# Kernel tuning notes

Hardware: AMD Instinct MI355X
Metric: run time of the kernel (lower is better)

## Reference

```python
import jax, jax.numpy as jnp
import numpy as np

NUM_GROUPS = 8
EPS = 1e-5


def group_norm(x, scale, bias):
    # x: [b, c, h, w]; 8 groups, affine, eps=1e-5 (torch GroupNorm defaults)
    b, c, h, w = x.shape
    xg = x.reshape(b, NUM_GROUPS, c // NUM_GROUPS * h * w)
    mean = jnp.mean(xg, axis=-1, keepdims=True)
    var = jnp.var(xg, axis=-1, keepdims=True)
    xg = (xg - mean) * jax.lax.rsqrt(var + EPS)
    x = xg.reshape(b, c, h, w)
    return x * scale[None, :, None, None] + bias[None, :, None, None]


def conv1x1(x, w, bias):
    # 1x1 conv == per-pixel linear: x [b,c,h,w], w [c_out,c_in], bias [c_out]
    return jnp.einsum('oc,bchw->bohw', w, x) + bias[None, :, None, None]


def setup_inputs() -> dict:
    key = jax.random.key(0)
    ks = jax.random.split(key, 11)
    b, c, h, w = 8, 512, 32, 32
    init = 1.0 / np.sqrt(c)
    d = {
        'x': jax.random.normal(ks[0], (b, c, h, w), dtype=jnp.float32),
        'gn_scale': jnp.ones((c,), jnp.float32),
        'gn_bias': jnp.zeros((c,), jnp.float32),
        'wq': jax.random.uniform(ks[1], (c, c), jnp.float32, -init, init),
        'bq': jax.random.uniform(ks[2], (c,), jnp.float32, -init, init),
        'wk': jax.random.uniform(ks[3], (c, c), jnp.float32, -init, init),
        'bk': jax.random.uniform(ks[4], (c,), jnp.float32, -init, init),
        'wv': jax.random.uniform(ks[5], (c, c), jnp.float32, -init, init),
        'bv': jax.random.uniform(ks[6], (c,), jnp.float32, -init, init),
        'wproj': jax.random.uniform(ks[7], (c, c), jnp.float32, -init, init),
        'bproj': jax.random.uniform(ks[8], (c,), jnp.float32, -init, init),
    }
    return d


def reference(x, gn_scale, gn_bias, wq, bq, wk, bk, wv, bv, wproj, bproj):
    b, c, h, w = x.shape
    h_ = group_norm(x, gn_scale, gn_bias)
    q = conv1x1(h_, wq, bq).reshape(b, c, h * w)  # [b,c,hw]
    k = conv1x1(h_, wk, bk).reshape(b, c, h * w)
    v = conv1x1(h_, wv, bv).reshape(b, c, h * w)
    scale = 1.0 / np.sqrt(c).astype(np.float32)
    # scores[b,i,j] = sum_c q[b,c,i]*k[b,c,j]
    scores = jnp.einsum('bci,bcj->bij', q, k) * scale
    attn = jax.nn.softmax(scores, axis=2)  # softmax over j (keys)
    # h_[b,c,i] = sum_j v[b,c,j] * attn[b,i,j]
    out = jnp.einsum('bcj,bij->bci', v, attn).reshape(b, c, h, w)
    out = conv1x1(out, wproj, bproj)
    return x + out
```

## Files before the change

### kernel.cpp

```cpp
#include <hip/hip_runtime.h>
#include <hip/hip_bf16.h>

#define DI __device__ __forceinline__

typedef __bf16 bf16x8 __attribute__((ext_vector_type(8)));
typedef float f32x4 __attribute__((ext_vector_type(4)));

typedef const void __attribute__((address_space(1))) gas_t;
typedef void __attribute__((address_space(3))) las_t;

DI unsigned short f2bf(float f) {
    unsigned u = __builtin_bit_cast(unsigned, f);
    u += 0x7fffu + ((u >> 16) & 1u);
    return (unsigned short)(u >> 16);
}

__global__ __launch_bounds__(256) void prep_kernel(const float* __restrict__ x,
                                                   float2* __restrict__ part,
                                                   const float* __restrict__ w0,
                                                   const float* __restrict__ w1,
                                                   const float* __restrict__ w2,
                                                   const float* __restrict__ w3,
                                                   unsigned short* __restrict__ wb) {
    int bx = blockIdx.x;
    int t = threadIdx.x;
    if (bx < 512) {
        int b = bx & 7, g = (bx >> 3) & 7, ch = bx >> 6;
        size_t base = ((size_t)b * 512 + g * 64 + ch * 8) * 1024;
        const float4* xp = (const float4*)(x + base);
        float s = 0.f, q = 0.f;
#pragma unroll
        for (int it = 0; it < 8; ++it) {
            float4 v = xp[it * 256 + t];
            s += (v.x + v.y) + (v.z + v.w);
            q += (v.x * v.x + v.y * v.y) + (v.z * v.z + v.w * v.w);
        }
#pragma unroll
        for (int o = 32; o; o >>= 1) { s += __shfl_xor(s, o); q += __shfl_xor(q, o); }
        __shared__ float rs[4], rq[4];
        int lane = t & 63, wid = t >> 6;
        if (!lane) { rs[wid] = s; rq[wid] = q; }
        __syncthreads();
        if (t == 0)
            part[((b * 8 + g) * 8) + ch] =
                make_float2(rs[0] + rs[1] + rs[2] + rs[3],
                            rq[0] + rq[1] + rq[2] + rq[3]);
    } else {
        int idx4 = bx - 512;
        int w = idx4 >> 8;
        const float* s = (w == 0) ? w0 : (w == 1) ? w1 : (w == 2) ? w2 : w3;
        unsigned short* o = wb + (size_t)w * 262144;
        int idx = (idx4 & 255) * 256 + t;
        float4 v = ((const float4*)s)[idx];
        ushort4 r;
        r.x = f2bf(v.x); r.y = f2bf(v.y); r.z = f2bf(v.z); r.w = f2bf(v.w);
        ((ushort4*)o)[idx] = r;
    }
}

__global__ __launch_bounds__(256) void gn_applyT(const float* __restrict__ x,
                                                 const float2* __restrict__ part,
                                                 const float* __restrict__ gs,
                                                 const float* __restrict__ gb,
                                                 unsigned short* __restrict__ hT) {
    int bx = blockIdx.x;
    int b = bx & 7, g = (bx >> 3) & 7, ic = bx >> 6;
    int bg = b * 8 + g;
    float s = 0.f, q = 0.f;
#pragma unroll
    for (int k = 0; k < 8; ++k) { float2 p = part[bg * 8 + k]; s += p.x; q += p.y; }
    float mean = s * (1.f / 65536.f);
    float var = q * (1.f / 65536.f) - mean * mean;
    float rstd = rsqrtf(var + 1e-5f);

    __shared__ unsigned short tile[128 * 66];
    int t = threadIdx.x;
    int i4 = t & 31, cq = t >> 5;
    size_t xbase = ((size_t)b * 512 + g * 64) * 1024 + ic * 128;
#pragma unroll
    for (int pass = 0; pass < 8; ++pass) {
        int c = pass * 8 + cq;
        float4 v = *(const float4*)&x[xbase + (size_t)c * 1024 + i4 * 4];
        int gc = g * 64 + c;
        float sc = gs[gc] * rstd, bi = gb[gc] - mean * sc;
        unsigned short* tp = &tile[(i4 * 4) * 66 + c];
        tp[0]   = f2bf(v.x * sc + bi);
        tp[66]  = f2bf(v.y * sc + bi);
        tp[132] = f2bf(v.z * sc + bi);
        tp[198] = f2bf(v.w * sc + bi);
    }
    __syncthreads();
    int i = t >> 1, h = t & 1;
    const unsigned short* tp2 = &tile[i * 66 + h * 32];
    unsigned short* op = &hT[(size_t)b * (1024 * 512) + (size_t)(ic * 128 + i) * 512 + g * 64 + h * 32];
#pragma unroll
    for (int cc = 0; cc < 4; ++cc) {
        unsigned short tmp[8];
#pragma unroll
        for (int j = 0; j < 8; ++j) tmp[j] = tp2[cc * 8 + j];
        *(uint4*)&op[cc * 8] = *(const uint4*)tmp;
    }
}

template <int ROWS>
DI void stage_tile(const unsigned short* __restrict__ g, int ldK,
                   unsigned short* lds, int t) {
    int row_in = t >> 3;
    int kg = (t & 7) ^ (row_in & 7);
    const unsigned short* src = g + (size_t)row_in * ldK + kg * 8;
    unsigned short* dst = lds + ((t >> 6) << 9);
#pragma unroll
    for (int c = 0; c < ROWS / 32; ++c) {
        __builtin_amdgcn_global_load_lds(
            (gas_t*)(unsigned long long)(src + (size_t)c * 32 * ldK),
            (las_t*)(unsigned)(unsigned long long)(dst + c * 2048),
            16, 0, 0);
    }
}

DI bf16x8 frag(const unsigned short* lds, int r, int kg) {
    return *(const bf16x8*)((const char*)lds + r * 128 + ((kg ^ (r & 7)) << 4));
}

template <int MR>
DI void compute_step(const unsigned short* As_, const unsigned short* Bs_,
                     f32x4 (&acc)[MR][4], int wm, int wn, int l15, int lks) {
#pragma unroll
    for (int kk = 0; kk < 2; ++kk) {
        bf16x8 a_[MR], b_[4];
#pragma unroll
        for (int m = 0; m < MR; ++m) a_[m] = frag(As_, wm + m * 16 + l15, kk * 4 + lks);
#pragma unroll
        for (int n = 0; n < 4; ++n) b_[n] = frag(Bs_, wn + n * 16 + l15, kk * 4 + lks);
#pragma unroll
        for (int m = 0; m < MR; ++m)
#pragma unroll
            for (int n = 0; n < 4; ++n)
                acc[m][n] = __builtin_amdgcn_mfma_f32_16x16x32_bf16(a_[m], b_[n], acc[m][n], 0, 0, 0);
    }
}

template <int TM, int MODE, int MINW, int PIPE>
__global__ __launch_bounds__(256, MINW) void gemm_bt(
        const unsigned short* __restrict__ A, const unsigned short* __restrict__ B,
        const float* __restrict__ b0, const float* __restrict__ b1,
        const float* __restrict__ b2,
        void* __restrict__ C0, void* __restrict__ C1, void* __restrict__ C2,
        const float* __restrict__ resid, float* __restrict__ spart,
        int M, int N, int K, float scale, size_t sA, size_t sB, size_t sC) {
    constexpr int MR = TM / 32;
    constexpr int NBUF = PIPE ? 2 : 1;
    __shared__ __align__(16) unsigned short As[NBUF][TM * 64];
    __shared__ __align__(16) unsigned short Bs[NBUF][128 * 64];
    int bx = blockIdx.x;
    int b = bx & 7;
    int tile = bx >> 3;
    int nTx = N >> 7;
    int tx = tile % nTx, ty = tile / nTx;
    int m0 = ty * TM, n0 = tx << 7;
    const unsigned short* Ag = A + sA * b + (size_t)m0 * K;
    const unsigned short* Bg = B + sB * b + (size_t)n0 * K;
    int t = threadIdx.x;
    int lane = t & 63, wid = t >> 6;
    int wm = (wid >> 1) * (TM / 2), wn = (wid & 1) * 64;
    const int l15 = lane & 15, lks = lane >> 4;

    f32x4 acc[MR][4];
#pragma unroll
    for (int i = 0; i < MR; ++i)
#pragma unroll
        for (int j = 0; j < 4; ++j) acc[i][j] = (f32x4){0.f, 0.f, 0.f, 0.f};

    float inv[4];
    if constexpr (MODE == 2) {
#pragma unroll
        for (int n = 0; n < 4; ++n) {
            int ng = n0 + wn + n * 16 + l15;
            float ssum = 0.f;
#pragma unroll
            for (int k = 0; k < 16; ++k) ssum += spart[(size_t)(b * 16 + k) * 1024 + ng];
            inv[n] = 1.f / ssum;
        }
    }
    float bn4[4];
    if constexpr (MODE == 3) {
#pragma unroll
        for (int n = 0; n < 4; ++n) bn4[n] = b0[n0 + wn + n * 16 + l15];
    }

    if constexpr (PIPE == 0) {
        for (int k0 = 0; k0 < K; k0 += 64) {
            stage_tile<TM>(Ag + k0, K, &As[0][0], t);
            stage_tile<128>(Bg + k0, K, &Bs[0][0], t);
            asm volatile("s_waitcnt vmcnt(0)" ::: "memory");
            __syncthreads();
            compute_step<MR>(&As[0][0], &Bs[0][0], acc, wm, wn, l15, lks);
            __syncthreads();
        }
    } else {
        stage_tile<TM>(Ag, K, &As[0][0], t);
        stage_tile<128>(Bg, K, &Bs[0][0], t);
        asm volatile("s_waitcnt vmcnt(0)" ::: "memory");
        __syncthreads();
        int cur = 0;
        for (int k0 = 0; k0 < K; k0 += 64) {
            if (k0 + 64 < K) {
                stage_tile<TM>(Ag + k0 + 64, K, &As[cur ^ 1][0], t);
                stage_tile<128>(Bg + k0 + 64, K, &Bs[cur ^ 1][0], t);
            }
            compute_step<MR>(&As[cur][0], &Bs[cur][0], acc, wm, wn, l15, lks);
            if (k0 + 64 < K) {
                asm volatile("s_waitcnt vmcnt(0)" ::: "memory");
                __syncthreads();
            }
            cur ^= 1;
        }
    }

    const int rbase = lks * 4;
    const size_t cb = sC * b;
    if constexpr (MODE == 0) {
        if (m0 < 1024) {
            unsigned short* Ct = (unsigned short*)(m0 < 512 ? C0 : C1) + cb;
            const float* bias = (m0 < 512) ? b0 : b1;
            int moff = (m0 < 512) ? 0 : 512;
#pragma unroll
            for (int m = 0; m < MR; ++m) {
                int mg = m0 - moff + wm + m * 16 + rbase;
                float bv4[4];
#pragma unroll
                for (int j = 0; j < 4; ++j) bv4[j] = bias[mg + j];
#pragma unroll
                for (int n = 0; n < 4; ++n) {
                    int ng = n0 + wn + n * 16 + l15;
                    f32x4 v = acc[m][n];
                    ushort4 o;
                    o.x = f2bf(v[0] + bv4[0]); o.y = f2bf(v[1] + bv4[1]);
                    o.z = f2bf(v[2] + bv4[2]); o.w = f2bf(v[3] + bv4[3]);
                    *(ushort4*)&Ct[(size_t)ng * 512 + mg] = o;
                }
            }
        } else {
            unsigned short* Vb = (unsigned short*)C2 + cb;
#pragma unroll
            for (int m = 0; m < MR; ++m) {
                int mg = m0 - 1024 + wm + m * 16 + rbase;
                float bv4[4];
#pragma unroll
                for (int j = 0; j < 4; ++j) bv4[j] = b2[mg + j];
#pragma unroll
                for (int n = 0; n < 4; ++n) {
                    int ng = n0 + wn + n * 16 + l15;
                    f32x4 v = acc[m][n];
#pragma unroll
                    for (int j = 0; j < 4; ++j)
                        Vb[(size_t)(mg + j) * 1024 + ng] = f2bf(v[j] + bv4[j]);
                }
            }
        }
    } else if constexpr (MODE == 1) {
        unsigned short* Ct = (unsigned short*)C0 + cb;
        float psum[4] = {0.f, 0.f, 0.f, 0.f};
#pragma unroll
        for (int m = 0; m < MR; ++m) {
            int mg = m0 + wm + m * 16 + rbase;
#pragma unroll
            for (int n = 0; n < 4; ++n) {
                int ng = n0 + wn + n * 16 + l15;
                f32x4 v = acc[m][n];
                float e0 = __expf(v[0] * scale), e1 = __expf(v[1] * scale);
                float e2 = __expf(v[2] * scale), e3 = __expf(v[3] * scale);
                psum[n] += (e0 + e1) + (e2 + e3);
                ushort4 o;
                o.x = f2bf(e0); o.y = f2bf(e1); o.z = f2bf(e2); o.w = f2bf(e3);
                *(ushort4*)&Ct[(size_t)ng * M + mg] = o;
            }
        }
        int rb = (m0 >> 7) * 2 + (wid >> 1);
#pragma unroll
        for (int n = 0; n < 4; ++n) {
            float p = psum[n];
            p += __shfl_xor(p, 16);
            p += __shfl_xor(p, 32);
            if (lks == 0) {
                int ng = n0 + wn + n * 16 + l15;
                spart[(size_t)(b * 16 + rb) * 1024 + ng] = p;
            }
        }
    } else if constexpr (MODE == 2) {
        unsigned short* Ct = (unsigned short*)C0 + cb;
#pragma unroll
        for (int m = 0; m < MR; ++m) {
            int mg = m0 + wm + m * 16 + rbase;
#pragma unroll
            for (int n = 0; n < 4; ++n) {
                int ng = n0 + wn + n * 16 + l15;
                f32x4 v = acc[m][n];
                ushort4 o;
                o.x = f2bf(v[0] * inv[n]); o.y = f2bf(v[1] * inv[n]);
                o.z = f2bf(v[2] * inv[n]); o.w = f2bf(v[3] * inv[n]);
                *(ushort4*)&Ct[(size_t)ng * M + mg] = o;
            }
        }
    } else {
        float* Cf = (float*)C0 + cb;
#pragma unroll
        for (int m = 0; m < MR; ++m) {
            int mg = m0 + wm + m * 16 + rbase;
#pragma unroll
            for (int n = 0; n < 4; ++n) {
                int ng = n0 + wn + n * 16 + l15;
                f32x4 v = acc[m][n];
                const float* rp = resid + cb + (size_t)ng * M + mg;
                float4 o;
                o.x = v[0] + bn4[n] + rp[0]; o.y = v[1] + bn4[n] + rp[1];
                o.z = v[2] + bn4[n] + rp[2]; o.w = v[3] + bn4[n] + rp[3];
                *(float4*)&Cf[(size_t)ng * M + mg] = o;
            }
        }
    }
}

extern "C" void kernel_launch(void* const* d_in, const int* in_sizes, int n_in,
                              void* d_out, int out_size, void* d_ws, size_t ws_size,
                              hipStream_t stream) {
    const float* x  = (const float*)d_in[0];
    const float* gs = (const float*)d_in[1];
    const float* gb = (const float*)d_in[2];
    const float* wq = (const float*)d_in[3];
    const float* bq = (const float*)d_in[4];
    const float* wk = (const float*)d_in[5];
    const float* bk = (const float*)d_in[6];
    const float* wv = (const float*)d_in[7];
    const float* bv = (const float*)d_in[8];
    const float* wp = (const float*)d_in[9];
    const float* bp = (const float*)d_in[10];
    float* out = (float*)d_out;

    char* ws = (char*)d_ws;
    const size_t MB = 1u << 20;
    unsigned short* hT = (unsigned short*)(ws + 0);
    unsigned short* wb = (unsigned short*)(ws + 8 * MB);
    unsigned short* qT = (unsigned short*)(ws + 10 * MB);
    unsigned short* kT = (unsigned short*)(ws + 18 * MB);
    unsigned short* vN = (unsigned short*)(ws + 26 * MB);
    unsigned short* E  = (unsigned short*)(ws + 34 * MB);
    unsigned short* OT = (unsigned short*)(ws + 50 * MB);
    float2* gnpart     = (float2*)(ws + 58 * MB);
    float*  spart      = (float*)(ws + 58 * MB + 65536);

    const unsigned short* wpb = wb + 3 * 262144;
    const size_t sH = 1024 * 512;
    const size_t sS = 1024 * 1024;

    prep_kernel<<<1536, 256, 0, stream>>>(x, gnpart, wq, wk, wv, wp, wb);
    gn_applyT<<<512, 256, 0, stream>>>(x, gnpart, gs, gb, hT);

    gemm_bt<128, 0, 3, 0><<<96 * 8, 256, 0, stream>>>(
        wb, hT, bq, bk, bv, qT, kT, vN, nullptr, nullptr,
        1536, 1024, 512, 1.f, 0, sH, sH);
    gemm_bt<128, 1, 2, 1><<<64 * 8, 256, 0, stream>>>(
        kT, qT, nullptr, nullptr, nullptr, E, nullptr, nullptr, nullptr, spart,
        1024, 1024, 512, 0.044194173824159216f, sH, sH, sS);
    gemm_bt<64, 2, 2, 1><<<64 * 8, 256, 0, stream>>>(
        vN, E, nullptr, nullptr, nullptr, OT, nullptr, nullptr, nullptr, spart,
        512, 1024, 1024, 1.f, sH, sS, sH);
    gemm_bt<64, 3, 2, 1><<<64 * 8, 256, 0, stream>>>(
        OT, wpb, bp, nullptr, nullptr, out, nullptr, nullptr, x, nullptr,
        1024, 512, 512, 1.f, sH, 0, (size_t)512 * 1024);
}
```

Baseline: 75.79 us.

## Fuse all stages into one cooperative persistent kernel with grid syncs

Replaces the six separate launches with a single cooperative kernel of 512 blocks that runs group-norm statistics with weight conversion, the normalize-transpose, and the four GEMM phases in sequence, separated by grid-wide barriers. The QKV projection is retiled to 192-row tiles so its work fits the fixed 512-block grid, and the weight conversion is folded into the stats blocks. The aim is to remove launch gaps and tail idle time between kernels. In exchange it adds grid-sync overhead, needs an occupancy of two blocks per CU, and limits each phase to the fixed grid size. The old multi-kernel path remains as a fallback.

```diff
diff --git a/kernel.cpp b/kernel.cpp
--- a/kernel.cpp
+++ b/kernel.cpp
@@ -1,5 +1,8 @@
 #include <hip/hip_runtime.h>
 #include <hip/hip_bf16.h>
+#include <hip/hip_cooperative_groups.h>
+
+namespace cg = cooperative_groups;
 
 #define DI __device__ __forceinline__
 
@@ -15,55 +18,258 @@
     return (unsigned short)(u >> 16);
 }
 
-__global__ __launch_bounds__(256) void prep_kernel(const float* __restrict__ x,
-                                                   float2* __restrict__ part,
-                                                   const float* __restrict__ w0,
-                                                   const float* __restrict__ w1,
-                                                   const float* __restrict__ w2,
-                                                   const float* __restrict__ w3,
-                                                   unsigned short* __restrict__ wb) {
-    int bx = blockIdx.x;
-    int t = threadIdx.x;
-    if (bx < 512) {
-        int b = bx & 7, g = (bx >> 3) & 7, ch = bx >> 6;
-        size_t base = ((size_t)b * 512 + g * 64 + ch * 8) * 1024;
-        const float4* xp = (const float4*)(x + base);
-        float s = 0.f, q = 0.f;
-#pragma unroll
-        for (int it = 0; it < 8; ++it) {
-            float4 v = xp[it * 256 + t];
-            s += (v.x + v.y) + (v.z + v.w);
-            q += (v.x * v.x + v.y * v.y) + (v.z * v.z + v.w * v.w);
-        }
-#pragma unroll
-        for (int o = 32; o; o >>= 1) { s += __shfl_xor(s, o); q += __shfl_xor(q, o); }
-        __shared__ float rs[4], rq[4];
-        int lane = t & 63, wid = t >> 6;
-        if (!lane) { rs[wid] = s; rq[wid] = q; }
+template <int ROWS>
+DI void stage_tile(const unsigned short* __restrict__ g, int ldK,
+                   unsigned short* lds, int t) {
+    int row_in = t >> 3;
+    int kg = (t & 7) ^ (row_in & 7);
+    const unsigned short* src = g + (size_t)row_in * ldK + kg * 8;
+    unsigned short* dst = lds + ((t >> 6) << 9);
+#pragma unroll
+    for (int c = 0; c < ROWS / 32; ++c) {
+        __builtin_amdgcn_global_load_lds(
+            (gas_t*)(unsigned long long)(src + (size_t)c * 32 * ldK),
+            (las_t*)(unsigned)(unsigned long long)(dst + c * 2048),
+            16, 0, 0);
+    }
+}
+
+DI bf16x8 frag(const unsigned short* lds, int r, int kg) {
+    return *(const bf16x8*)((const char*)lds + r * 128 + ((kg ^ (r & 7)) << 4));
+}
+
+template <int MR>
+DI void compute_step(const unsigned short* As_, const unsigned short* Bs_,
+                     f32x4 (&acc)[MR][4], int wm, int wn, int l15, int lks) {
+#pragma unroll
+    for (int kk = 0; kk < 2; ++kk) {
+        bf16x8 a_[MR], b_[4];
+#pragma unroll
+        for (int m = 0; m < MR; ++m) a_[m] = frag(As_, wm + m * 16 + l15, kk * 4 + lks);
+#pragma unroll
+        for (int n = 0; n < 4; ++n) b_[n] = frag(Bs_, wn + n * 16 + l15, kk * 4 + lks);
+#pragma unroll
+        for (int m = 0; m < MR; ++m)
+#pragma unroll
+            for (int n = 0; n < 4; ++n)
+                acc[m][n] = __builtin_amdgcn_mfma_f32_16x16x32_bf16(a_[m], b_[n], acc[m][n], 0, 0, 0);
+    }
+}
+
+template <int TM, int MODE, int PIPE>
+DI void gemm_phase(unsigned short* AsB, unsigned short* BsB,
+                   const unsigned short* __restrict__ A, const unsigned short* __restrict__ B,
+                   const float* __restrict__ b0, const float* __restrict__ b1,
+                   const float* __restrict__ b2,
+                   void* __restrict__ C0, void* __restrict__ C1, void* __restrict__ C2,
+                   const float* __restrict__ resid, float* __restrict__ spart,
+                   int M, int N, int K, float scale, size_t sA, size_t sB, size_t sC,
+                   int bx, int t) {
+    constexpr int MR = TM / 32;
+    constexpr int ABUF = TM * 64;
+    constexpr int BBUF = 128 * 64;
+    int b = bx & 7;
+    int tile = bx >> 3;
+    int nTx = N >> 7;
+    int tx = tile % nTx, ty = tile / nTx;
+    int m0 = ty * TM, n0 = tx << 7;
+    const unsigned short* Ag = A + sA * b + (size_t)m0 * K;
+    const unsigned short* Bg = B + sB * b + (size_t)n0 * K;
+    int lane = t & 63, wid = t >> 6;
+    int wm = (wid >> 1) * (TM / 2), wn = (wid & 1) * 64;
+    const int l15 = lane & 15, lks = lane >> 4;
+
+    f32x4 acc[MR][4];
+#pragma unroll
+    for (int i = 0; i < MR; ++i)
+#pragma unroll
+        for (int j = 0; j < 4; ++j) acc[i][j] = (f32x4){0.f, 0.f, 0.f, 0.f};
+
+    float inv[4];
+    if constexpr (MODE == 2) {
+#pragma unroll
+        for (int n = 0; n < 4; ++n) {
+            int ng = n0 + wn + n * 16 + l15;
+            float ssum = 0.f;
+#pragma unroll
+            for (int k = 0; k < 16; ++k) ssum += spart[(size_t)(b * 16 + k) * 1024 + ng];
+            inv[n] = 1.f / ssum;
+        }
+    }
+    float bn4[4];
+    if constexpr (MODE == 3) {
+#pragma unroll
+        for (int n = 0; n < 4; ++n) bn4[n] = b0[n0 + wn + n * 16 + l15];
+    }
+
+    if constexpr (PIPE == 0) {
+        for (int k0 = 0; k0 < K; k0 += 64) {
+            stage_tile<TM>(Ag + k0, K, AsB, t);
+            stage_tile<128>(Bg + k0, K, BsB, t);
+            asm volatile("s_waitcnt vmcnt(0)" ::: "memory");
+            __syncthreads();
+            compute_step<MR>(AsB, BsB, acc, wm, wn, l15, lks);
+            __syncthreads();
+        }
+    } else {
+        stage_tile<TM>(Ag, K, AsB, t);
+        stage_tile<128>(Bg, K, BsB, t);
+        asm volatile("s_waitcnt vmcnt(0)" ::: "memory");
         __syncthreads();
-        if (t == 0)
-            part[((b * 8 + g) * 8) + ch] =
-                make_float2(rs[0] + rs[1] + rs[2] + rs[3],
-                            rq[0] + rq[1] + rq[2] + rq[3]);
+        int cur = 0;
+        for (int k0 = 0; k0 < K; k0 += 64) {
+            if (k0 + 64 < K) {
+                stage_tile<TM>(Ag + k0 + 64, K, AsB + (cur ^ 1) * ABUF, t);
+                stage_tile<128>(Bg + k0 + 64, K, BsB + (cur ^ 1) * BBUF, t);
+            }
+            compute_step<MR>(AsB + cur * ABUF, BsB + cur * BBUF, acc, wm, wn, l15, lks);
+            if (k0 + 64 < K) {
+                asm volatile("s_waitcnt vmcnt(0)" ::: "memory");
+                __syncthreads();
+            }
+            cur ^= 1;
+        }
+    }
+
+    const int rbase = lks * 4;
+    const size_t cb = sC * b;
+    if constexpr (MODE == 0) {
+#pragma unroll
+        for (int m = 0; m < MR; ++m) {
+            int mgg = m0 + wm + m * 16 + rbase;
+            int region = mgg >> 9;
+            int local = mgg & 511;
+            const float* bias = (region == 0) ? b0 : (region == 1) ? b1 : b2;
+            float bv4[4];
+#pragma unroll
+            for (int j = 0; j < 4; ++j) bv4[j] = bias[local + j];
+            if (region < 2) {
+                unsigned short* Ct = (unsigned short*)(region == 0 ? C0 : C1) + cb;
+#pragma unroll
+                for (int n = 0; n < 4; ++n) {
+                    int ng = n0 + wn + n * 16 + l15;
+                    f32x4 v = acc[m][n];
+                    ushort4 o;
+                    o.x = f2bf(v[0] + bv4[0]); o.y = f2bf(v[1] + bv4[1]);
+                    o.z = f2bf(v[2] + bv4[2]); o.w = f2bf(v[3] + bv4[3]);
+                    *(ushort4*)&Ct[(size_t)ng * 512 + local] = o;
+                }
+            } else {
+                unsigned short* Vb = (unsigned short*)C2 + cb;
+#pragma unroll
+                for (int n = 0; n < 4; ++n) {
+                    int ng = n0 + wn + n * 16 + l15;
+                    f32x4 v = acc[m][n];
+#pragma unroll
+                    for (int j = 0; j < 4; ++j)
+                        Vb[(size_t)(local + j) * 1024 + ng] = f2bf(v[j] + bv4[j]);
+                }
+            }
+        }
+    } else if constexpr (MODE == 1) {
+        unsigned short* Ct = (unsigned short*)C0 + cb;
+        float psum[4] = {0.f, 0.f, 0.f, 0.f};
+#pragma unroll
+        for (int m = 0; m < MR; ++m) {
+            int mg = m0 + wm + m * 16 + rbase;
+#pragma unroll
+            for (int n = 0; n < 4; ++n) {
+                int ng = n0 + wn + n * 16 + l15;
+                f32x4 v = acc[m][n];
+                float e0 = __expf(v[0] * scale), e1 = __expf(v[1] * scale);
+                float e2 = __expf(v[2] * scale), e3 = __expf(v[3] * scale);
+                psum[n] += (e0 + e1) + (e2 + e3);
+                ushort4 o;
+                o.x = f2bf(e0); o.y = f2bf(e1); o.z = f2bf(e2); o.w = f2bf(e3);
+                *(ushort4*)&Ct[(size_t)ng * M + mg] = o;
+            }
+        }
+        int rb = (m0 >> 7) * 2 + (wid >> 1);
+#pragma unroll
+        for (int n = 0; n < 4; ++n) {
+            float p = psum[n];
+            p += __shfl_xor(p, 16);
+            p += __shfl_xor(p, 32);
+            if (lks == 0) {
+                int ng = n0 + wn + n * 16 + l15;
+                spart[(size_t)(b * 16 + rb) * 1024 + ng] = p;
+            }
+        }
+    } else if constexpr (MODE == 2) {
+        unsigned short* Ct = (unsigned short*)C0 + cb;
+#pragma unroll
+        for (int m = 0; m < MR; ++m) {
+            int mg = m0 + wm + m * 16 + rbase;
+#pragma unroll
+            for (int n = 0; n < 4; ++n) {
+                int ng = n0 + wn + n * 16 + l15;
+                f32x4 v = acc[m][n];
+                ushort4 o;
+                o.x = f2bf(v[0] * inv[n]); o.y = f2bf(v[1] * inv[n]);
+                o.z = f2bf(v[2] * inv[n]); o.w = f2bf(v[3] * inv[n]);
+                *(ushort4*)&Ct[(size_t)ng * M + mg] = o;
+            }
+        }
     } else {
-        int idx4 = bx - 512;
-        int w = idx4 >> 8;
-        const float* s = (w == 0) ? w0 : (w == 1) ? w1 : (w == 2) ? w2 : w3;
+        float* Cf = (float*)C0 + cb;
+#pragma unroll
+        for (int m = 0; m < MR; ++m) {
+            int mg = m0 + wm + m * 16 + rbase;
+#pragma unroll
+            for (int n = 0; n < 4; ++n) {
+                int ng = n0 + wn + n * 16 + l15;
+                f32x4 v = acc[m][n];
+                const float* rp = resid + cb + (size_t)ng * M + mg;
+                float4 o;
+                o.x = v[0] + bn4[n] + rp[0]; o.y = v[1] + bn4[n] + rp[1];
+                o.z = v[2] + bn4[n] + rp[2]; o.w = v[3] + bn4[n] + rp[3];
+                *(float4*)&Cf[(size_t)ng * M + mg] = o;
+            }
+        }
+    }
+}
+
+DI void stats_wcvt_body(const float* __restrict__ x, float2* __restrict__ part,
+                        const float* __restrict__ w0, const float* __restrict__ w1,
+                        const float* __restrict__ w2, const float* __restrict__ w3,
+                        unsigned short* __restrict__ wb, float* red,
+                        int bx, int t, int nchunk) {
+    int b = bx & 7, g = (bx >> 3) & 7, ch = bx >> 6;
+    size_t base = ((size_t)b * 512 + g * 64 + ch * 8) * 1024;
+    const float4* xp = (const float4*)(x + base);
+    float s = 0.f, q = 0.f;
+#pragma unroll
+    for (int it = 0; it < 8; ++it) {
+        float4 v = xp[it * 256 + t];
+        s += (v.x + v.y) + (v.z + v.w);
+        q += (v.x * v.x + v.y * v.y) + (v.z * v.z + v.w * v.w);
+    }
+#pragma unroll
+    for (int o = 32; o; o >>= 1) { s += __shfl_xor(s, o); q += __shfl_xor(q, o); }
+    int lane = t & 63, wid = t >> 6;
+    if (!lane) { red[wid] = s; red[4 + wid] = q; }
+    __syncthreads();
+    if (t == 0)
+        part[((b * 8 + g) * 8) + ch] =
+            make_float2(red[0] + red[1] + red[2] + red[3],
+                        red[4] + red[5] + red[6] + red[7]);
+    for (int cc = 0; cc < nchunk; ++cc) {
+        int chunk = bx * nchunk + cc;
+        int w = chunk >> 8;
+        const float* sp = (w == 0) ? w0 : (w == 1) ? w1 : (w == 2) ? w2 : w3;
         unsigned short* o = wb + (size_t)w * 262144;
-        int idx = (idx4 & 255) * 256 + t;
-        float4 v = ((const float4*)s)[idx];
+        int idx = (chunk & 255) * 256 + t;
+        float4 v = ((const float4*)sp)[idx];
         ushort4 r;
         r.x = f2bf(v.x); r.y = f2bf(v.y); r.z = f2bf(v.z); r.w = f2bf(v.w);
         ((ushort4*)o)[idx] = r;
     }
 }
 
-__global__ __launch_bounds__(256) void gn_applyT(const float* __restrict__ x,
-                                                 const float2* __restrict__ part,
-                                                 const float* __restrict__ gs,
-                                                 const float* __restrict__ gb,
-                                                 unsigned short* __restrict__ hT) {
-    int bx = blockIdx.x;
+DI void gn_apply_body(const float* __restrict__ x, const float2* __restrict__ part,
+                      const float* __restrict__ gs, const float* __restrict__ gb,
+                      unsigned short* __restrict__ hT, unsigned short* tile,
+                      int bx, int t) {
     int b = bx & 7, g = (bx >> 3) & 7, ic = bx >> 6;
     int bg = b * 8 + g;
     float s = 0.f, q = 0.f;
@@ -73,8 +279,6 @@
     float var = q * (1.f / 65536.f) - mean * mean;
     float rstd = rsqrtf(var + 1e-5f);
 
-    __shared__ unsigned short tile[128 * 66];
-    int t = threadIdx.x;
     int i4 = t & 31, cq = t >> 5;
     size_t xbase = ((size_t)b * 512 + g * 64) * 1024 + ic * 128;
 #pragma unroll
@@ -102,42 +306,73 @@
     }
 }
 
-template <int ROWS>
-DI void stage_tile(const unsigned short* __restrict__ g, int ldK,
-                   unsigned short* lds, int t) {
-    int row_in = t >> 3;
-    int kg = (t & 7) ^ (row_in & 7);
-    const unsigned short* src = g + (size_t)row_in * ldK + kg * 8;
-    unsigned short* dst = lds + ((t >> 6) << 9);
-#pragma unroll
-    for (int c = 0; c < ROWS / 32; ++c) {
-        __builtin_amdgcn_global_load_lds(
-            (gas_t*)(unsigned long long)(src + (size_t)c * 32 * ldK),
-            (las_t*)(unsigned)(unsigned long long)(dst + c * 2048),
-            16, 0, 0);
-    }
-}
-
-DI bf16x8 frag(const unsigned short* lds, int r, int kg) {
-    return *(const bf16x8*)((const char*)lds + r * 128 + ((kg ^ (r & 7)) << 4));
-}
-
-template <int MR>
-DI void compute_step(const unsigned short* As_, const unsigned short* Bs_,
-                     f32x4 (&acc)[MR][4], int wm, int wn, int l15, int lks) {
-#pragma unroll
-    for (int kk = 0; kk < 2; ++kk) {
-        bf16x8 a_[MR], b_[4];
-#pragma unroll
-        for (int m = 0; m < MR; ++m) a_[m] = frag(As_, wm + m * 16 + l15, kk * 4 + lks);
-#pragma unroll
-        for (int n = 0; n < 4; ++n) b_[n] = frag(Bs_, wn + n * 16 + l15, kk * 4 + lks);
-#pragma unroll
-        for (int m = 0; m < MR; ++m)
-#pragma unroll
-            for (int n = 0; n < 4; ++n)
-                acc[m][n] = __builtin_amdgcn_mfma_f32_16x16x32_bf16(a_[m], b_[n], acc[m][n], 0, 0, 0);
-    }
+struct Params {
+    const float *x, *gs, *gb, *wq, *bq, *wk, *bk, *wv, *bv, *wp, *bp;
+    float* out;
+    unsigned short *hT, *wb, *qT, *kT, *vN, *E, *OT;
+    float2* gnpart;
+    float* spart;
+};
+
+__global__ __launch_bounds__(256, 2) void fused_kernel(Params p) {
+    __shared__ __align__(16) unsigned short smem[32768];
+    cg::grid_group grid = cg::this_grid();
+    int bx = blockIdx.x, t = threadIdx.x;
+    const size_t sH = 1024 * 512;
+    const size_t sS = 1024 * 1024;
+
+    stats_wcvt_body(p.x, p.gnpart, p.wq, p.wk, p.wv, p.wp, p.wb, (float*)smem, bx, t, 2);
+    grid.sync();
+    gn_apply_body(p.x, p.gnpart, p.gs, p.gb, p.hT, smem, bx, t);
+    grid.sync();
+    gemm_phase<192, 0, 0>(smem, smem + 12288, p.wb, p.hT, p.bq, p.bk, p.bv,
+                          p.qT, p.kT, p.vN, nullptr, nullptr,
+                          1536, 1024, 512, 1.f, 0, sH, sH, bx, t);
+    grid.sync();
+    gemm_phase<128, 1, 1>(smem, smem + 16384, p.kT, p.qT, nullptr, nullptr, nullptr,
+                          p.E, nullptr, nullptr, nullptr, p.spart,
+                          1024, 1024, 512, 0.044194173824159216f, sH, sH, sS, bx, t);
+    grid.sync();
+    gemm_phase<64, 2, 1>(smem, smem + 8192, p.vN, p.E, nullptr, nullptr, nullptr,
+                         p.OT, nullptr, nullptr, nullptr, p.spart,
+                         512, 1024, 1024, 1.f, sH, sS, sH, bx, t);
+    grid.sync();
+    gemm_phase<64, 3, 1>(smem, smem + 8192, p.OT, p.wb + 3 * 262144, p.bp, nullptr, nullptr,
+                         p.out, nullptr, nullptr, p.x, nullptr,
+                         1024, 512, 512, 1.f, sH, 0, sH, bx, t);
+}
+
+__global__ __launch_bounds__(256) void prep_kernel(const float* __restrict__ x,
+                                                   float2* __restrict__ part,
+                                                   const float* __restrict__ w0,
+                                                   const float* __restrict__ w1,
+                                                   const float* __restrict__ w2,
+                                                   const float* __restrict__ w3,
+                                                   unsigned short* __restrict__ wb) {
+    __shared__ float red[8];
+    int bx = blockIdx.x, t = threadIdx.x;
+    if (bx < 512) {
+        stats_wcvt_body(x, part, w0, w1, w2, w3, wb, red, bx, t, 0);
+    } else {
+        int chunk = bx - 512;
+        int w = chunk >> 8;
+        const float* sp = (w == 0) ? w0 : (w == 1) ? w1 : (w == 2) ? w2 : w3;
+        unsigned short* o = wb + (size_t)w * 262144;
+        int idx = (chunk & 255) * 256 + t;
+        float4 v = ((const float4*)sp)[idx];
+        ushort4 r;
+        r.x = f2bf(v.x); r.y = f2bf(v.y); r.z = f2bf(v.z); r.w = f2bf(v.w);
+        ((ushort4*)o)[idx] = r;
+    }
+}
+
+__global__ __launch_bounds__(256) void gn_applyT(const float* __restrict__ x,
+                                                 const float2* __restrict__ part,
+                                                 const float* __restrict__ gs,
+                                                 const float* __restrict__ gb,
+                                                 unsigned short* __restrict__ hT) {
+    __shared__ unsigned short tile[128 * 66];
+    gn_apply_body(x, part, gs, gb, hT, tile, blockIdx.x, threadIdx.x);
 }
 
 template <int TM, int MODE, int MINW, int PIPE>
@@ -148,177 +383,11 @@
         void* __restrict__ C0, void* __restrict__ C1, void* __restrict__ C2,
         const float* __restrict__ resid, float* __restrict__ spart,
         int M, int N, int K, float scale, size_t sA, size_t sB, size_t sC) {
-    constexpr int MR = TM / 32;
     constexpr int NBUF = PIPE ? 2 : 1;
-    __shared__ __align__(16) unsigned short As[NBUF][TM * 64];
-    __shared__ __align__(16) unsigned short Bs[NBUF][128 * 64];
-    int bx = blockIdx.x;
-    int b = bx & 7;
-    int tile = bx >> 3;
-    int nTx = N >> 7;
-    int tx = tile % nTx, ty = tile / nTx;
-    int m0 = ty * TM, n0 = tx << 7;
-    const unsigned short* Ag = A + sA * b + (size_t)m0 * K;
-    const unsigned short* Bg = B + sB * b + (size_t)n0 * K;
-    int t = threadIdx.x;
-    int lane = t & 63, wid = t >> 6;
-    int wm = (wid >> 1) * (TM / 2), wn = (wid & 1) * 64;
-    const int l15 = lane & 15, lks = lane >> 4;
-
-    f32x4 acc[MR][4];
-#pragma unroll
-    for (int i = 0; i < MR; ++i)
-#pragma unroll
-        for (int j = 0; j < 4; ++j) acc[i][j] = (f32x4){0.f, 0.f, 0.f, 0.f};
-
-    float inv[4];
-    if constexpr (MODE == 2) {
-#pragma unroll
-        for (int n = 0; n < 4; ++n) {
-            int ng = n0 + wn + n * 16 + l15;
-            float ssum = 0.f;
-#pragma unroll
-            for (int k = 0; k < 16; ++k) ssum += spart[(size_t)(b * 16 + k) * 1024 + ng];
-            inv[n] = 1.f / ssum;
-        }
-    }
-    float bn4[4];
-    if constexpr (MODE == 3) {
-#pragma unroll
-        for (int n = 0; n < 4; ++n) bn4[n] = b0[n0 + wn + n * 16 + l15];
-    }
-
-    if constexpr (PIPE == 0) {
-        for (int k0 = 0; k0 < K; k0 += 64) {
-            stage_tile<TM>(Ag + k0, K, &As[0][0], t);
-            stage_tile<128>(Bg + k0, K, &Bs[0][0], t);
-            asm volatile("s_waitcnt vmcnt(0)" ::: "memory");
-            __syncthreads();
-            compute_step<MR>(&As[0][0], &Bs[0][0], acc, wm, wn, l15, lks);
-            __syncthreads();
-        }
-    } else {
-        stage_tile<TM>(Ag, K, &As[0][0], t);
-        stage_tile<128>(Bg, K, &Bs[0][0], t);
-        asm volatile("s_waitcnt vmcnt(0)" ::: "memory");
-        __syncthreads();
-        int cur = 0;
-        for (int k0 = 0; k0 < K; k0 += 64) {
-            if (k0 + 64 < K) {
-                stage_tile<TM>(Ag + k0 + 64, K, &As[cur ^ 1][0], t);
-                stage_tile<128>(Bg + k0 + 64, K, &Bs[cur ^ 1][0], t);
-            }
-            compute_step<MR>(&As[cur][0], &Bs[cur][0], acc, wm, wn, l15, lks);
-            if (k0 + 64 < K) {
-                asm volatile("s_waitcnt vmcnt(0)" ::: "memory");
-                __syncthreads();
-            }
-            cur ^= 1;
-        }
-    }
-
-    const int rbase = lks * 4;
-    const size_t cb = sC * b;
-    if constexpr (MODE == 0) {
-        if (m0 < 1024) {
-            unsigned short* Ct = (unsigned short*)(m0 < 512 ? C0 : C1) + cb;
-            const float* bias = (m0 < 512) ? b0 : b1;
-            int moff = (m0 < 512) ? 0 : 512;
-#pragma unroll
-            for (int m = 0; m < MR; ++m) {
-                int mg = m0 - moff + wm + m * 16 + rbase;
-                float bv4[4];
-#pragma unroll
-                for (int j = 0; j < 4; ++j) bv4[j] = bias[mg + j];
-#pragma unroll
-                for (int n = 0; n < 4; ++n) {
-                    int ng = n0 + wn + n * 16 + l15;
-                    f32x4 v = acc[m][n];
-                    ushort4 o;
-                    o.x = f2bf(v[0] + bv4[0]); o.y = f2bf(v[1] + bv4[1]);
-                    o.z = f2bf(v[2] + bv4[2]); o.w = f2bf(v[3] + bv4[3]);
-                    *(ushort4*)&Ct[(size_t)ng * 512 + mg] = o;
-                }
-            }
-        } else {
-            unsigned short* Vb = (unsigned short*)C2 + cb;
-#pragma unroll
-            for (int m = 0; m < MR; ++m) {
-                int mg = m0 - 1024 + wm + m * 16 + rbase;
-                float bv4[4];
-#pragma unroll
-                for (int j = 0; j < 4; ++j) bv4[j] = b2[mg + j];
-#pragma unroll
-                for (int n = 0; n < 4; ++n) {
-                    int ng = n0 + wn + n * 16 + l15;
-                    f32x4 v = acc[m][n];
-#pragma unroll
-                    for (int j = 0; j < 4; ++j)
-                        Vb[(size_t)(mg + j) * 1024 + ng] = f2bf(v[j] + bv4[j]);
-                }
-            }
-        }
-    } else if constexpr (MODE == 1) {
-        unsigned short* Ct = (unsigned short*)C0 + cb;
-        float psum[4] = {0.f, 0.f, 0.f, 0.f};
-#pragma unroll
-        for (int m = 0; m < MR; ++m) {
-            int mg = m0 + wm + m * 16 + rbase;
-#pragma unroll
-            for (int n = 0; n < 4; ++n) {
-                int ng = n0 + wn + n * 16 + l15;
-                f32x4 v = acc[m][n];
-                float e0 = __expf(v[0] * scale), e1 = __expf(v[1] * scale);
-                float e2 = __expf(v[2] * scale), e3 = __expf(v[3] * scale);
-                psum[n] += (e0 + e1) + (e2 + e3);
-                ushort4 o;
-                o.x = f2bf(e0); o.y = f2bf(e1); o.z = f2bf(e2); o.w = f2bf(e3);
-                *(ushort4*)&Ct[(size_t)ng * M + mg] = o;
-            }
-        }
-        int rb = (m0 >> 7) * 2 + (wid >> 1);
-#pragma unroll
-        for (int n = 0; n < 4; ++n) {
-            float p = psum[n];
-            p += __shfl_xor(p, 16);
-            p += __shfl_xor(p, 32);
-            if (lks == 0) {
-                int ng = n0 + wn + n * 16 + l15;
-                spart[(size_t)(b * 16 + rb) * 1024 + ng] = p;
-            }
-        }
-    } else if constexpr (MODE == 2) {
-        unsigned short* Ct = (unsigned short*)C0 + cb;
-#pragma unroll
-        for (int m = 0; m < MR; ++m) {
-            int mg = m0 + wm + m * 16 + rbase;
-#pragma unroll
-            for (int n = 0; n < 4; ++n) {
-                int ng = n0 + wn + n * 16 + l15;
-                f32x4 v = acc[m][n];
-                ushort4 o;
-                o.x = f2bf(v[0] * inv[n]); o.y = f2bf(v[1] * inv[n]);
-                o.z = f2bf(v[2] * inv[n]); o.w = f2bf(v[3] * inv[n]);
-                *(ushort4*)&Ct[(size_t)ng * M + mg] = o;
-            }
-        }
-    } else {
-        float* Cf = (float*)C0 + cb;
-#pragma unroll
-        for (int m = 0; m < MR; ++m) {
-            int mg = m0 + wm + m * 16 + rbase;
-#pragma unroll
-            for (int n = 0; n < 4; ++n) {
-                int ng = n0 + wn + n * 16 + l15;
-                f32x4 v = acc[m][n];
-                const float* rp = resid + cb + (size_t)ng * M + mg;
-                float4 o;
-                o.x = v[0] + bn4[n] + rp[0]; o.y = v[1] + bn4[n] + rp[1];
-                o.z = v[2] + bn4[n] + rp[2]; o.w = v[3] + bn4[n] + rp[3];
-                *(float4*)&Cf[(size_t)ng * M + mg] = o;
-            }
-        }
-    }
+    __shared__ __align__(16) unsigned short As[NBUF * TM * 64];
+    __shared__ __align__(16) unsigned short Bs[NBUF * 128 * 64];
+    gemm_phase<TM, MODE, PIPE>(As, Bs, A, B, b0, b1, b2, C0, C1, C2, resid, spart,
+                               M, N, K, scale, sA, sB, sC, blockIdx.x, threadIdx.x);
 }
 
 extern "C" void kernel_launch(void* const* d_in, const int* in_sizes, int n_in,
@@ -353,9 +422,27 @@
     const size_t sH = 1024 * 512;
     const size_t sS = 1024 * 1024;
 
+    int dev = 0;
+    (void)hipGetDevice(&dev);
+    int coop = 0;
+    (void)hipDeviceGetAttribute(&coop, hipDeviceAttributeCooperativeLaunch, dev);
+    int maxB = 0;
+    (void)hipOccupancyMaxActiveBlocksPerMultiprocessor(&maxB, fused_kernel, 256, 0);
+    if (coop && maxB >= 2) {
+        Params p;
+        p.x = x; p.gs = gs; p.gb = gb; p.wq = wq; p.bq = bq; p.wk = wk; p.bk = bk;
+        p.wv = wv; p.bv = bv; p.wp = wp; p.bp = bp; p.out = out;
+        p.hT = hT; p.wb = wb; p.qT = qT; p.kT = kT; p.vN = vN; p.E = E; p.OT = OT;
+        p.gnpart = gnpart; p.spart = spart;
+        void* args[] = {&p};
+        hipError_t rc = hipLaunchCooperativeKernel(fused_kernel, dim3(512), dim3(256),
+                                                   args, 0u, stream);
+        if (rc == hipSuccess) return;
+        (void)hipGetLastError();
+    }
+
     prep_kernel<<<1536, 256, 0, stream>>>(x, gnpart, wq, wk, wv, wp, wb);
     gn_applyT<<<512, 256, 0, stream>>>(x, gnpart, gs, gb, hT);
-
     gemm_bt<128, 0, 3, 0><<<96 * 8, 256, 0, stream>>>(
         wb, hT, bq, bk, bv, qT, kT, vN, nullptr, nullptr,
         1536, 1024, 512, 1.f, 0, sH, sH);
@@ -367,5 +454,5 @@
         512, 1024, 1024, 1.f, sH, sS, sH);
     gemm_bt<64, 3, 2, 1><<<64 * 8, 256, 0, stream>>>(
         OT, wpb, bp, nullptr, nullptr, out, nullptr, nullptr, x, nullptr,
-        1024, 512, 512, 1.f, sH, 0, (size_t)512 * 1024);
-}
+        1024, 512, 512, 1.f, sH, 0, sH);
+}
```

Measured after the change: 75.87 us. No clear change (+0.1%).
